# Performance work log

Measured on AMD Instinct MI355X. Metric: run time of the kernel, lower is better.

The kernel has to match this reference:

```python
import jax, jax.numpy as jnp
import numpy as np

B, A, D = 256, 128, 5          # batch, max_atoms, max_degree
FA, FB, C = 256, 64, 256       # atom feats, bond feats, conv_width


def setup_inputs() -> dict:
    key = jax.random.key(0)
    k1, k2, k3, k4 = jax.random.split(key, 4)
    atoms = jax.random.normal(k1, (B, A, FA), dtype=jnp.float32)
    bonds = jax.random.normal(k2, (B, A, D, FB), dtype=jnp.float32)
    # neighbour indices with -1 as padding value
    edges = jax.random.randint(k3, (B, A, D), -1, A, dtype=jnp.int32)
    W = jax.random.normal(k4, (D, FA + FB, C), dtype=jnp.float32) * 0.05
    b = jnp.zeros((D, C), dtype=jnp.float32)
    return {"atoms": atoms, "bonds": bonds, "edges": edges, "W": W, "b": b}


def reference(atoms, bonds, edges, W, b):
    # atom degree = number of non-padding neighbours  (B, A)
    deg = jnp.sum(edges != -1, axis=-1)

    # neighbour_lookup: pad a zero atom at index 0, shift indices by +1 so -1 -> 0
    masked_atoms = jnp.pad(atoms, ((0, 0), (1, 0), (0, 0)))        # (B, A+1, FA)
    idx = edges + 1                                                # (B, A, D)
    neigh = masked_atoms[jnp.arange(B)[:, None, None], idx]        # (B, A, D, FA)

    # include_self=True then sum over neighbour axis == self + sum(neighbours)
    summed_atom = atoms + jnp.sum(neigh, axis=2)                   # (B, A, FA)
    summed_bond = jnp.sum(bonds, axis=2)                           # (B, A, FB)
    feat = jnp.concatenate([summed_atom, summed_bond], axis=-1)    # (B, A, FA+FB)

    # per-degree Dense (relu), masked by (degree == d), summed over degrees
    dense = jax.nn.relu(jnp.einsum('baf,dfc->badc', feat, W) + b)  # (B, A, D, C)
    mask = (deg[..., None] == jnp.arange(D)).astype(dense.dtype)   # (B, A, D)
    return jnp.einsum('badc,bad->bac', dense, mask)                # (B, A, C)
```

## Files before the change

### kernel.cpp

```cpp
#include <hip/hip_runtime.h>


#define NB 256
#define NA 128
#define ND 5
#define NFA 256
#define NFB 64
#define NC 256
#define NF (NFA + NFB)
#define NROWS (NB * NA)
#define RPB 64
#define RPC 8
#define NBLK (NROWS / RPB)

__global__ __launch_bounds__(256) void ngh_fused_kernel(
    const float* __restrict__ atoms,
    const float* __restrict__ bonds,
    const int*   __restrict__ edges,
    const float* __restrict__ W,
    const float* __restrict__ bias,
    float* __restrict__ out)
{
    __shared__ float feat[NF * RPC];
    __shared__ int   cnt_s[ND];
    __shared__ int   lists[ND][RPB];
    const int t  = threadIdx.x;
    const int r0 = blockIdx.x * RPB;

    if (t < ND) cnt_s[t] = 0;

    float4* dst = reinterpret_cast<float4*>(out + (size_t)r0 * NC);
    const float4 z = make_float4(0.f, 0.f, 0.f, 0.f);
#pragma unroll
    for (int k = 0; k < (RPB * NC / 4) / 256; ++k) dst[t + k * 256] = z;

    __syncthreads();

    if (t < RPB) {
        const int row = r0 + t;
        const int* er = edges + row * ND;
        int deg = 0;
#pragma unroll
        for (int d = 0; d < ND; ++d) deg += (er[d] != -1) ? 1 : 0;
        if (deg < ND) {
            const int p = atomicAdd(&cnt_s[deg], 1);
            lists[deg][p] = row;
        }
    }
    __syncthreads();

    for (int d = 0; d < ND; ++d) {
        const int n = cnt_s[d];
        for (int j0 = 0; j0 < n; j0 += RPC) {
            const int nr = min(RPC, n - j0);
            int rows_r[RPC];
#pragma unroll
            for (int r = 0; r < RPC; ++r)
                rows_r[r] = (r < nr) ? lists[d][j0 + r] : -1;

#pragma unroll
            for (int r = 0; r < RPC; ++r) {
                const int row = rows_r[r];
                float v = 0.f;
                if (row >= 0) {
                    const int rb = row & ~(NA - 1);
                    const int* er = edges + row * ND;
                    v = atoms[(size_t)row * NFA + t];
#pragma unroll
                    for (int dd = 0; dd < ND; ++dd) {
                        const int e = er[dd];
                        if (e != -1) v += atoms[(size_t)(rb + e) * NFA + t];
                    }
                }
                feat[t * RPC + r] = v;
                if (t < NFB) {
                    float bs = 0.f;
                    if (row >= 0) {
                        const float* br = bonds + (size_t)row * (ND * NFB) + t;
#pragma unroll
                        for (int dd = 0; dd < ND; ++dd) bs += br[dd * NFB];
                    }
                    feat[(NFA + t) * RPC + r] = bs;
                }
            }
            __syncthreads();

            const float* Wd = W + (size_t)d * (NF * NC) + t;
            const float bv = bias[d * NC + t];
            float acc[RPC];
#pragma unroll
            for (int r = 0; r < RPC; ++r) acc[r] = bv;
#pragma unroll 4
            for (int f = 0; f < NF; ++f) {
                const float w = Wd[(size_t)f * NC];
                const float4 p0 = *reinterpret_cast<const float4*>(&feat[f * RPC]);
                const float4 p1 = *reinterpret_cast<const float4*>(&feat[f * RPC + 4]);
                acc[0] = fmaf(p0.x, w, acc[0]);
                acc[1] = fmaf(p0.y, w, acc[1]);
                acc[2] = fmaf(p0.z, w, acc[2]);
                acc[3] = fmaf(p0.w, w, acc[3]);
                acc[4] = fmaf(p1.x, w, acc[4]);
                acc[5] = fmaf(p1.y, w, acc[5]);
                acc[6] = fmaf(p1.z, w, acc[6]);
                acc[7] = fmaf(p1.w, w, acc[7]);
            }
#pragma unroll
            for (int r = 0; r < RPC; ++r)
                if (rows_r[r] >= 0)
                    out[(size_t)rows_r[r] * NC + t] = fmaxf(acc[r], 0.f);
            __syncthreads();
        }
    }
}

extern "C" void kernel_launch(void* const* d_in, const int* in_sizes, int n_in,
                              void* d_out, int out_size, void* d_ws, size_t ws_size,
                              hipStream_t stream) {
    const float* atoms = (const float*)d_in[0];
    const float* bonds = (const float*)d_in[1];
    const int*   edges = (const int*)  d_in[2];
    const float* W     = (const float*)d_in[3];
    const float* bias  = (const float*)d_in[4];
    float*       out   = (float*)d_out;

    ngh_fused_kernel<<<dim3(NBLK), dim3(256), 0, stream>>>(
        atoms, bonds, edges, W, bias, out);
}
```

Baseline: 150.9 us.

## Split K across waves with float4 W loads and LDS reduction; 128-row blocks

Blocks now hold 512 threads over 128 rows. The GEMM is split along the feature dimension across 8 waves: each lane computes 4 output columns with float4 W loads, and the partial sums are reduced through shared memory before bias and ReLU are applied. Edges are staged in LDS, and only rows whose degree is 5 (which would otherwise get no output) are zero-filled, which avoids writing every output row twice. The cost is an extra LDS reduction pass with more barriers per group, lower per-thread arithmetic intensity on W, and fewer blocks in the grid.

```diff
diff --git a/kernel.cpp b/kernel.cpp
--- a/kernel.cpp
+++ b/kernel.cpp
@@ -9,11 +9,21 @@
 #define NC 256
 #define NF (NFA + NFB)
 #define NROWS (NB * NA)
-#define RPB 64
-#define RPC 8
+#define RPB 128
 #define NBLK (NROWS / RPB)
+#define NT 512
+#define G 8
+#define FPW (NF / 8)
 
-__global__ __launch_bounds__(256) void ngh_fused_kernel(
+__device__ __forceinline__ float4 fma4(float s, float4 wv, float4 a) {
+    a.x = fmaf(s, wv.x, a.x);
+    a.y = fmaf(s, wv.y, a.y);
+    a.z = fmaf(s, wv.z, a.z);
+    a.w = fmaf(s, wv.w, a.w);
+    return a;
+}
+
+__global__ __launch_bounds__(NT) void ngh_kernel(
     const float* __restrict__ atoms,
     const float* __restrict__ bonds,
     const int*   __restrict__ edges,
@@ -21,93 +31,139 @@
     const float* __restrict__ bias,
     float* __restrict__ out)
 {
-    __shared__ float feat[NF * RPC];
-    __shared__ int   cnt_s[ND];
-    __shared__ int   lists[ND][RPB];
+    __shared__ int eds[RPB * ND];
+    __shared__ int cnt_s[ND];
+    __shared__ int lists[ND][RPB];
+    __shared__ unsigned mask[4];
+    __shared__ int rows_s[G];
+    __shared__ alignas(16) float  feat[NF * G];
+    __shared__ alignas(16) float4 red[8][G][64];
+
     const int t  = threadIdx.x;
     const int r0 = blockIdx.x * RPB;
+    const int w  = t >> 6;
+    const int l  = t & 63;
 
     if (t < ND) cnt_s[t] = 0;
+    if (t < 4)  mask[t]  = 0u;
 
-    float4* dst = reinterpret_cast<float4*>(out + (size_t)r0 * NC);
-    const float4 z = make_float4(0.f, 0.f, 0.f, 0.f);
-#pragma unroll
-    for (int k = 0; k < (RPB * NC / 4) / 256; ++k) dst[t + k * 256] = z;
-
+    eds[t] = edges[r0 * ND + t];
+    if (t < RPB * ND - NT) eds[NT + t] = edges[r0 * ND + NT + t];
     __syncthreads();
 
     if (t < RPB) {
-        const int row = r0 + t;
-        const int* er = edges + row * ND;
-        int deg = 0;
+        int dg = 0;
 #pragma unroll
-        for (int d = 0; d < ND; ++d) deg += (er[d] != -1) ? 1 : 0;
-        if (deg < ND) {
-            const int p = atomicAdd(&cnt_s[deg], 1);
-            lists[deg][p] = row;
+        for (int d = 0; d < ND; ++d) dg += (eds[t * ND + d] != -1) ? 1 : 0;
+        if (dg < ND) {
+            const int p = atomicAdd(&cnt_s[dg], 1);
+            lists[dg][p] = t;
+            atomicOr(&mask[t >> 5], 1u << (t & 31));
         }
     }
     __syncthreads();
 
+    {
+        float4* o4 = reinterpret_cast<float4*>(out + (size_t)r0 * NC);
+        const float4 z = make_float4(0.f, 0.f, 0.f, 0.f);
+#pragma unroll
+        for (int k = 0; k < (RPB * NC / 4) / NT; ++k) {
+            const int i  = t + k * NT;
+            const int lr = i >> 6;
+            if (!((mask[lr >> 5] >> (lr & 31)) & 1u)) o4[i] = z;
+        }
+    }
+
     for (int d = 0; d < ND; ++d) {
         const int n = cnt_s[d];
-        for (int j0 = 0; j0 < n; j0 += RPC) {
-            const int nr = min(RPC, n - j0);
-            int rows_r[RPC];
+        for (int j0 = 0; j0 < n; j0 += G) {
+            const int nr = min(G, n - j0);
+            if (t < G) rows_s[t] = (t < nr) ? lists[d][j0 + t] : -1;
+            __syncthreads();
+
+            if (t < NFA) {
 #pragma unroll
-            for (int r = 0; r < RPC; ++r)
-                rows_r[r] = (r < nr) ? lists[d][j0 + r] : -1;
-
+                for (int r = 0; r < G; ++r) {
+                    const int lrow = rows_s[r];
+                    float v = 0.f;
+                    if (lrow >= 0) {
+                        const int row = r0 + lrow;
+                        const int rb  = row & ~(NA - 1);
+                        v = atoms[(size_t)row * NFA + t];
 #pragma unroll
-            for (int r = 0; r < RPC; ++r) {
-                const int row = rows_r[r];
-                float v = 0.f;
-                if (row >= 0) {
-                    const int rb = row & ~(NA - 1);
-                    const int* er = edges + row * ND;
-                    v = atoms[(size_t)row * NFA + t];
+                        for (int dd = 0; dd < ND; ++dd) {
+                            const int e = eds[lrow * ND + dd];
+                            if (e != -1) v += atoms[(size_t)(rb + e) * NFA + t];
+                        }
+                    }
+                    feat[t * G + r] = v;
+                }
+            } else if (t < NFA + NFB) {
+                const int f = t - NFA;
 #pragma unroll
-                    for (int dd = 0; dd < ND; ++dd) {
-                        const int e = er[dd];
-                        if (e != -1) v += atoms[(size_t)(rb + e) * NFA + t];
+                for (int r = 0; r < G; ++r) {
+                    const int lrow = rows_s[r];
+                    float v = 0.f;
+                    if (lrow >= 0) {
+                        const float* br = bonds + (size_t)(r0 + lrow) * (ND * NFB) + f;
+#pragma unroll
+                        for (int dd = 0; dd < ND; ++dd) v += br[dd * NFB];
                     }
-                }
-                feat[t * RPC + r] = v;
-                if (t < NFB) {
-                    float bs = 0.f;
-                    if (row >= 0) {
-                        const float* br = bonds + (size_t)row * (ND * NFB) + t;
-#pragma unroll
-                        for (int dd = 0; dd < ND; ++dd) bs += br[dd * NFB];
-                    }
-                    feat[(NFA + t) * RPC + r] = bs;
+                    feat[(NFA + f) * G + r] = v;
                 }
             }
             __syncthreads();
 
-            const float* Wd = W + (size_t)d * (NF * NC) + t;
-            const float bv = bias[d * NC + t];
-            float acc[RPC];
+            float4 acc[G];
 #pragma unroll
-            for (int r = 0; r < RPC; ++r) acc[r] = bv;
+            for (int r = 0; r < G; ++r) acc[r] = make_float4(0.f, 0.f, 0.f, 0.f);
+            {
+                const float4* f4 = reinterpret_cast<const float4*>(feat);
+                const float*  Wd = W + (size_t)d * (NF * NC);
+                const int fbase = w * FPW;
 #pragma unroll 4
-            for (int f = 0; f < NF; ++f) {
-                const float w = Wd[(size_t)f * NC];
-                const float4 p0 = *reinterpret_cast<const float4*>(&feat[f * RPC]);
-                const float4 p1 = *reinterpret_cast<const float4*>(&feat[f * RPC + 4]);
-                acc[0] = fmaf(p0.x, w, acc[0]);
-                acc[1] = fmaf(p0.y, w, acc[1]);
-                acc[2] = fmaf(p0.z, w, acc[2]);
-                acc[3] = fmaf(p0.w, w, acc[3]);
-                acc[4] = fmaf(p1.x, w, acc[4]);
-                acc[5] = fmaf(p1.y, w, acc[5]);
-                acc[6] = fmaf(p1.z, w, acc[6]);
-                acc[7] = fmaf(p1.w, w, acc[7]);
+                for (int fi = 0; fi < FPW; ++fi) {
+                    const int f = fbase + fi;
+                    const float4 wv = *reinterpret_cast<const float4*>(
+                        &Wd[(size_t)f * NC + l * 4]);
+                    const float4 p0 = f4[f * 2];
+                    const float4 p1 = f4[f * 2 + 1];
+                    acc[0] = fma4(p0.x, wv, acc[0]);
+                    acc[1] = fma4(p0.y, wv, acc[1]);
+                    acc[2] = fma4(p0.z, wv, acc[2]);
+                    acc[3] = fma4(p0.w, wv, acc[3]);
+                    acc[4] = fma4(p1.x, wv, acc[4]);
+                    acc[5] = fma4(p1.y, wv, acc[5]);
+                    acc[6] = fma4(p1.z, wv, acc[6]);
+                    acc[7] = fma4(p1.w, wv, acc[7]);
+                }
             }
 #pragma unroll
-            for (int r = 0; r < RPC; ++r)
-                if (rows_r[r] >= 0)
-                    out[(size_t)rows_r[r] * NC + t] = fmaxf(acc[r], 0.f);
+            for (int r = 0; r < G; ++r) red[w][r][l] = acc[r];
+            __syncthreads();
+
+            {
+                const int r    = t >> 6;
+                const int li   = t & 63;
+                const int lrow = rows_s[r];
+                if (lrow >= 0) {
+                    float4 s = red[0][r][li];
+#pragma unroll
+                    for (int wi = 1; wi < 8; ++wi) {
+                        const float4 q = red[wi][r][li];
+                        s.x += q.x; s.y += q.y; s.z += q.z; s.w += q.w;
+                    }
+                    const float4 bv = *reinterpret_cast<const float4*>(
+                        &bias[d * NC + li * 4]);
+                    float4 o;
+                    o.x = fmaxf(s.x + bv.x, 0.f);
+                    o.y = fmaxf(s.y + bv.y, 0.f);
+                    o.z = fmaxf(s.z + bv.z, 0.f);
+                    o.w = fmaxf(s.w + bv.w, 0.f);
+                    *reinterpret_cast<float4*>(
+                        &out[(size_t)(r0 + lrow) * NC + li * 4]) = o;
+                }
+            }
             __syncthreads();
         }
     }
@@ -123,6 +179,6 @@
     const float* bias  = (const float*)d_in[4];
     float*       out   = (float*)d_out;
 
-    ngh_fused_kernel<<<dim3(NBLK), dim3(256), 0, stream>>>(
+    ngh_kernel<<<dim3(NBLK), dim3(NT), 0, stream>>>(
         atoms, bonds, edges, W, bias, out);
 }
```

After: 134.8 us. -10.7%, faster.
